# Kernel tuning notes

Hardware: AMD Instinct MI355X
Metric: run time of the kernel (lower is better)

The kernel has to match this reference:

```python
import jax, jax.numpy as jnp
import numpy as np

N = 50000        # nodes
E = 800000       # edges
F_IN = 32        # float features (x also carries 1 trailing cell-id column)
CELL_DIM = 16
NUM_CELLS = 854
C = 64           # out_channels
H0, H1 = 2, 1    # heads schedule for num_layers=2 -> [2, 1]
D_IN = F_IN + CELL_DIM  # 48, GAT input dim after cell embedding concat
NEG_SLOPE = 0.2  # PyG GATConv default negative_slope


def setup_inputs() -> dict:
    key = jax.random.key(0)
    ks = jax.random.split(key, 14)
    base = jax.random.normal(ks[0], (N, F_IN), jnp.float32)
    cell_ids = jax.random.randint(ks[1], (N,), 0, NUM_CELLS)
    x = jnp.concatenate([base, cell_ids.astype(jnp.float32)[:, None]], axis=1)
    edge_index = jax.random.randint(ks[2], (2, E), 0, N, dtype=jnp.int32)
    s = lambda f: 1.0 / np.sqrt(f)
    emb = jax.random.normal(ks[3], (NUM_CELLS, CELL_DIM), jnp.float32)
    W0 = jax.random.normal(ks[4], (D_IN, H0 * C), jnp.float32) * s(D_IN)
    a_src0 = jax.random.normal(ks[5], (H0, C), jnp.float32) * s(C)
    a_dst0 = jax.random.normal(ks[6], (H0, C), jnp.float32) * s(C)
    b0 = jnp.zeros((C,), jnp.float32)
    ln_g = jnp.ones((C,), jnp.float32)
    ln_b = jnp.zeros((C,), jnp.float32)
    W1 = jax.random.normal(ks[7], (C, H1 * C), jnp.float32) * s(C)
    a_src1 = jax.random.normal(ks[8], (H1, C), jnp.float32) * s(C)
    a_dst1 = jax.random.normal(ks[9], (H1, C), jnp.float32) * s(C)
    b1 = jnp.zeros((C,), jnp.float32)
    return {"x": x, "edge_index": edge_index, "emb": emb,
            "W0": W0, "a_src0": a_src0, "a_dst0": a_dst0, "b0": b0,
            "ln_g": ln_g, "ln_b": ln_b,
            "W1": W1, "a_src1": a_src1, "a_dst1": a_dst1, "b1": b1}


def gat_layer(h_in, src, dst, W, a_src, a_dst, b, heads):
    # h_in: [N, D]; src/dst: [E'] (self-loops already appended)
    h = (h_in @ W).reshape(N, heads, C)                 # [N, H, C]
    alpha_s = jnp.einsum('nhc,hc->nh', h, a_src)        # [N, H]
    alpha_d = jnp.einsum('nhc,hc->nh', h, a_dst)
    e = jax.nn.leaky_relu(alpha_s[src] + alpha_d[dst], NEG_SLOPE)  # [E', H]
    # segment softmax over incoming edges of each dst node
    m = jax.ops.segment_max(e, dst, num_segments=N)     # [N, H]
    ex = jnp.exp(e - m[dst])
    denom = jax.ops.segment_sum(ex, dst, num_segments=N)
    alpha = ex / denom[dst]                             # [E', H]
    msg = h[src] * alpha[:, :, None]                    # [E', H, C]
    out = jax.ops.segment_sum(msg, dst, num_segments=N) # [N, H, C]
    return out.mean(axis=1) + b                         # concat=False -> mean over heads


def layer_norm(x, g, b):
    mu = x.mean(-1, keepdims=True)
    var = ((x - mu) ** 2).mean(-1, keepdims=True)
    return (x - mu) * jax.lax.rsqrt(var + 1e-5) * g + b


def reference(x, edge_index, emb, W0, a_src0, a_dst0, b0, ln_g, ln_b,
              W1, a_src1, a_dst1, b1):
    base = x[:, :-1]
    cell_ids = x[:, -1].astype(jnp.int32)
    h = jnp.concatenate([base, emb[cell_ids]], axis=1)  # [N, 48]
    # add self-loops (PyG GATConv default add_self_loops=True)
    loop = jnp.arange(N, dtype=edge_index.dtype)
    src = jnp.concatenate([edge_index[0], loop])
    dst = jnp.concatenate([edge_index[1], loop])
    h = gat_layer(h, src, dst, W0, a_src0, a_dst0, b0, H0)
    h = jax.nn.elu(layer_norm(h, ln_g, ln_b))           # dropout is identity at eval
    h = gat_layer(h, src, dst, W1, a_src1, a_dst1, b1, H1)
    return h
```

## Files before the change

kernel.cpp:

```cpp
#include <hip/hip_runtime.h>
#include <hip/hip_bf16.h>

#define N_NODES 50000
#define N_EDGES 800000
#define F_IN 32
#define CELL_DIM 16
#define D_IN 48
#define X_STRIDE 33
#define NUM_CELLS 854
#define NEG_SLOPE 0.2f
#define NODE0_BLOCKS 2048
#define EDGE_BLOCKS 3125
#define NXCD 8
#define BWX 16
#define W 24

typedef unsigned int uint;
typedef unsigned short ushort;

static __device__ __forceinline__ uint f2b(float f) {
  uint x = __float_as_uint(f);
  return (x + 0x7fffu + ((x >> 16) & 1u)) >> 16;
}
static __device__ __forceinline__ float b2f_lo(uint w) { return __uint_as_float(w << 16); }
static __device__ __forceinline__ float b2f_hi(uint w) { return __uint_as_float(w & 0xffff0000u); }
static __device__ __forceinline__ float lrelu(float e) { return fmaxf(e, NEG_SLOPE * e); }


__global__ __launch_bounds__(256) void k_node0(const float* __restrict__ x,
                                               const float* __restrict__ emb,
                                               const float* __restrict__ W0,
                                               const float* __restrict__ asrc,
                                               const float* __restrict__ adst,
                                               ushort* __restrict__ h0u,
                                               float* __restrict__ as0, float* __restrict__ ad0) {
  int tid = threadIdx.x;
  __shared__ float hin[8][48];
  int lane = tid & 63, wid = tid >> 6;
  int h = wid & 1;
  int q = wid >> 1;
  float w0r[D_IN];
#pragma unroll
  for (int k = 0; k < D_IN; ++k) w0r[k] = W0[k * 128 + h * 64 + lane];
  float av_s = asrc[h * 64 + lane], av_d = adst[h * 64 + lane];

  for (int g = blockIdx.x; g < N_NODES / 8; g += NODE0_BLOCKS) {
    int nb = g * 8;
#pragma unroll
    for (int j = 0; j < 2; ++j) {
      int loc = 2 * wid + j;
      int n = nb + loc;
      float t = 0.f;
      if (lane < 33) t = x[n * X_STRIDE + lane];
      int cid = (int)__shfl(t, 32, 64);
      cid = cid < 0 ? 0 : (cid >= NUM_CELLS ? NUM_CELLS - 1 : cid);
      if (lane >= 32 && lane < 48) t = emb[cid * CELL_DIM + (lane - 32)];
      if (lane < 48) hin[loc][lane] = t;
    }
    __syncthreads();
#pragma unroll
    for (int j = 0; j < 4; ++j) {
      int loc = 4 * q + j;
      int n = nb + loc;
      const float4* hp = (const float4*)hin[loc];
      float acc = 0.f;
#pragma unroll
      for (int k4 = 0; k4 < 12; ++k4) {
        float4 hh = hp[k4];
        acc = fmaf(hh.x, w0r[4 * k4 + 0], acc);
        acc = fmaf(hh.y, w0r[4 * k4 + 1], acc);
        acc = fmaf(hh.z, w0r[4 * k4 + 2], acc);
        acc = fmaf(hh.w, w0r[4 * k4 + 3], acc);
      }
      h0u[(n * 64 + lane) * 2 + h] = (ushort)f2b(acc);
      float sa = acc * av_s, sd = acc * av_d;
#pragma unroll
      for (int o = 32; o >= 1; o >>= 1) {
        sa += __shfl_xor(sa, o, 64);
        sd += __shfl_xor(sd, o, 64);
      }
      if (lane == 0) {
        as0[n * 2 + h] = sa;
        ad0[n * 2 + h] = sd;
      }
    }
    __syncthreads();
  }
}


__global__ __launch_bounds__(256) void k_bfill(const int* __restrict__ ei,
                                               int* __restrict__ cnt,
                                               ushort* __restrict__ bkt) {
  int e = blockIdx.x * 256 + threadIdx.x;
  if (e >= N_EDGES) return;
  uint xcc;
  asm volatile("s_getreg_b32 %0, hwreg(HW_REG_XCC_ID)" : "=s"(xcc));
  xcc &= (NXCD - 1);
  int s = ei[e], d = ei[N_EDGES + e];
  int p = atomicAdd(&cnt[xcc * N_NODES + d], 1);
  if (p < BWX) bkt[(xcc * N_NODES + d) * BWX + p] = (ushort)s;
}



__global__ __launch_bounds__(256) void k_agg0(const int* __restrict__ cnt,
                                              const ushort* __restrict__ bkt,
                                              const float2* __restrict__ as0v,
                                              const float2* __restrict__ ad0v,
                                              const uint* __restrict__ h0p,
                                              const float* __restrict__ b0,
                                              const float* __restrict__ lng,
                                              const float* __restrict__ lnb,
                                              const float* __restrict__ W1,
                                              const float* __restrict__ asrc1,
                                              const float* __restrict__ adst1,
                                              ushort* __restrict__ h1b,
                                              float* __restrict__ as1, float* __restrict__ ad1) {
  __shared__ uint gbuf[4][W * 64];
  __shared__ float yb[4][64];
  int tid = threadIdx.x;
  int lane = tid & 63, wl = tid >> 6;
  int n = blockIdx.x * 4 + wl;
  int cx = 0;
  if (lane < 8) cx = min(cnt[lane * N_NODES + n], BWX);
  int sc = cx;
#pragma unroll
  for (int o = 1; o < 8; o <<= 1) {
    int t = __shfl_up(sc, o, 64);
    if (lane >= o) sc += t;
  }
  int p1 = __shfl(sc, 0, 64), p2 = __shfl(sc, 1, 64), p3 = __shfl(sc, 2, 64);
  int p4 = __shfl(sc, 3, 64), p5 = __shfl(sc, 4, 64), p6 = __shfl(sc, 5, 64);
  int p7 = __shfl(sc, 6, 64);
  int total = __shfl(sc, 7, 64);
  int items = total + 1;

  float2 ad = ad0v[n];
  float acc0 = 0.f, acc1 = 0.f, den0 = 0.f, den1 = 0.f;
  uint* gb = gbuf[wl];

  for (int w0 = 0; w0 < items; w0 += W) {
    int idx = w0 + lane;
    int xsl = (idx >= p1) + (idx >= p2) + (idx >= p3) + (idx >= p4) +
              (idx >= p5) + (idx >= p6) + (idx >= p7);
    int base = xsl == 0 ? 0 : (xsl == 1 ? p1 : (xsl == 2 ? p2 : (xsl == 3 ? p3 :
               (xsl == 4 ? p4 : (xsl == 5 ? p5 : (xsl == 6 ? p6 : p7))))));
    uint sl = (uint)bkt[xsl * (N_NODES * BWX) + n * BWX + (idx - base)];
    uint s = (idx < total) ? sl : (uint)n;
    float wv0 = 0.f, wv1 = 0.f;
    if (lane < W && idx < items) {
      float2 a = as0v[s];
      wv0 = __expf(lrelu(a.x + ad.x));
      wv1 = __expf(lrelu(a.y + ad.y));
    }
#pragma unroll
    for (int j = 0; j < W; ++j) {
      uint sx = (uint)__builtin_amdgcn_readlane((int)s, j);
      __builtin_amdgcn_global_load_lds((const uint*)(h0p + sx * 64u + (uint)lane),
                                       gb + j * 64, 4, 0, 0);
    }
    asm volatile("s_waitcnt vmcnt(0)" ::: "memory");
    __builtin_amdgcn_sched_barrier(0);
#pragma unroll
    for (int j = 0; j < W; ++j) {
      float w0j = __uint_as_float(
          (uint)__builtin_amdgcn_readlane((int)__float_as_uint(wv0), j));
      float w1j = __uint_as_float(
          (uint)__builtin_amdgcn_readlane((int)__float_as_uint(wv1), j));
      uint h = gb[j * 64 + lane];
      acc0 = fmaf(w0j, b2f_lo(h), acc0); den0 += w0j;
      acc1 = fmaf(w1j, b2f_hi(h), acc1); den1 += w1j;
    }
    asm volatile("s_waitcnt lgkmcnt(0)" ::: "memory");
    __builtin_amdgcn_sched_barrier(0);
  }

  float v = 0.5f * (acc0 / den0 + acc1 / den1) + b0[lane];
  float mu = v;
#pragma unroll
  for (int o = 32; o >= 1; o >>= 1) mu += __shfl_xor(mu, o, 64);
  mu *= (1.0f / 64.0f);
  float d = v - mu;
  float vr = d * d;
#pragma unroll
  for (int o = 32; o >= 1; o >>= 1) vr += __shfl_xor(vr, o, 64);
  vr *= (1.0f / 64.0f);
  float y = d * rsqrtf(vr + 1e-5f) * lng[lane] + lnb[lane];
  y = y > 0.f ? y : expm1f(y);
  yb[wl][lane] = y;
  const float4* yp = (const float4*)yb[wl];
  float q0 = 0.f, q1 = 0.f, q2 = 0.f, q3 = 0.f;
#pragma unroll
  for (int k4 = 0; k4 < 16; ++k4) {
    float4 yy = yp[k4];
    q0 = fmaf(yy.x, W1[(4 * k4 + 0) * 64 + lane], q0);
    q1 = fmaf(yy.y, W1[(4 * k4 + 1) * 64 + lane], q1);
    q2 = fmaf(yy.z, W1[(4 * k4 + 2) * 64 + lane], q2);
    q3 = fmaf(yy.w, W1[(4 * k4 + 3) * 64 + lane], q3);
  }
  float h1v = (q0 + q1) + (q2 + q3);
  h1b[n * 64 + lane] = (ushort)f2b(h1v);
  float sa = h1v * asrc1[lane];
  float sdv = h1v * adst1[lane];
#pragma unroll
  for (int o = 32; o >= 1; o >>= 1) {
    sa += __shfl_xor(sa, o, 64);
    sdv += __shfl_xor(sdv, o, 64);
  }
  if (lane == 0) {
    as1[n] = sa;
    ad1[n] = sdv;
  }
}


__global__ __launch_bounds__(256) void k_agg1(const int* __restrict__ cnt,
                                              const ushort* __restrict__ bkt,
                                              const ushort* __restrict__ h1b,
                                              const float* __restrict__ as1,
                                              const float* __restrict__ ad1,
                                              const float* __restrict__ b1,
                                              float* __restrict__ out) {
  __shared__ uint gbuf[4][W * 64];
  int tid = threadIdx.x;
  int lane = tid & 63, wl = tid >> 6;
  int n = blockIdx.x * 4 + wl;
  int cx = 0;
  if (lane < 8) cx = min(cnt[lane * N_NODES + n], BWX);
  int sc = cx;
#pragma unroll
  for (int o = 1; o < 8; o <<= 1) {
    int t = __shfl_up(sc, o, 64);
    if (lane >= o) sc += t;
  }
  int p1 = __shfl(sc, 0, 64), p2 = __shfl(sc, 1, 64), p3 = __shfl(sc, 2, 64);
  int p4 = __shfl(sc, 3, 64), p5 = __shfl(sc, 4, 64), p6 = __shfl(sc, 5, 64);
  int p7 = __shfl(sc, 6, 64);
  int total = __shfl(sc, 7, 64);
  int items = total + 1;

  float adv = ad1[n];
  float acc = 0.f, den = 0.f;
  uint* gb = gbuf[wl];
  const ushort* gbs = (const ushort*)gb;

  for (int w0 = 0; w0 < items; w0 += W) {
    int idx = w0 + lane;
    int xsl = (idx >= p1) + (idx >= p2) + (idx >= p3) + (idx >= p4) +
              (idx >= p5) + (idx >= p6) + (idx >= p7);
    int base = xsl == 0 ? 0 : (xsl == 1 ? p1 : (xsl == 2 ? p2 : (xsl == 3 ? p3 :
               (xsl == 4 ? p4 : (xsl == 5 ? p5 : (xsl == 6 ? p6 : p7))))));
    uint sl = (uint)bkt[xsl * (N_NODES * BWX) + n * BWX + (idx - base)];
    uint s = (idx < total) ? sl : (uint)n;
    float wv = 0.f;
    if (lane < W && idx < items) {
      wv = __expf(lrelu(as1[s] + adv));
    }
    uint hl = lane & 31;
#pragma unroll
    for (int j = 0; j < W; ++j) {
      uint sx = (uint)__builtin_amdgcn_readlane((int)s, j);
      __builtin_amdgcn_global_load_lds((const uint*)(h1b + sx * 64u) + hl,
                                       gb + j * 64, 4, 0, 0);
    }
    asm volatile("s_waitcnt vmcnt(0)" ::: "memory");
    __builtin_amdgcn_sched_barrier(0);
#pragma unroll
    for (int j = 0; j < W; ++j) {
      float wj = __uint_as_float(
          (uint)__builtin_amdgcn_readlane((int)__float_as_uint(wv), j));
      uint hh = (uint)gbs[j * 128 + lane];
      acc = fmaf(wj, __uint_as_float(hh << 16), acc);
      den += wj;
    }
    asm volatile("s_waitcnt lgkmcnt(0)" ::: "memory");
    __builtin_amdgcn_sched_barrier(0);
  }
  out[n * 64 + lane] = acc / den + b1[lane];
}


extern "C" void kernel_launch(void* const* d_in, const int* in_sizes, int n_in,
                              void* d_out, int out_size, void* d_ws, size_t ws_size,
                              hipStream_t stream) {
  const float* x    = (const float*)d_in[0];
  const int*   ei   = (const int*)d_in[1];
  const float* emb  = (const float*)d_in[2];
  const float* W0   = (const float*)d_in[3];
  const float* as0w = (const float*)d_in[4];
  const float* ad0w = (const float*)d_in[5];
  const float* b0   = (const float*)d_in[6];
  const float* lng  = (const float*)d_in[7];
  const float* lnb  = (const float*)d_in[8];
  const float* W1   = (const float*)d_in[9];
  const float* as1w = (const float*)d_in[10];
  const float* ad1w = (const float*)d_in[11];
  const float* b1   = (const float*)d_in[12];
  float* out = (float*)d_out;

  ushort* bkt = (ushort*)d_ws;
  int* cnt   = (int*)(bkt + NXCD * N_NODES * BWX);
  float* as0 = (float*)(cnt + NXCD * N_NODES);
  float* ad0 = as0 + N_NODES * 2;
  float* as1 = ad0 + N_NODES * 2;
  float* ad1 = as1 + N_NODES;
  uint* h0p  = (uint*)(ad1 + N_NODES);
  ushort* h1b = (ushort*)(h0p + N_NODES * 64);

  hipMemsetAsync(cnt, 0, NXCD * N_NODES * sizeof(int), stream);
  k_bfill<<<EDGE_BLOCKS, 256, 0, stream>>>(ei, cnt, bkt);
  k_node0<<<NODE0_BLOCKS, 256, 0, stream>>>(x, emb, W0, as0w, ad0w, (ushort*)h0p, as0, ad0);
  k_agg0<<<N_NODES / 4, 256, 0, stream>>>(cnt, bkt, (const float2*)as0, (const float2*)ad0,
                                          h0p, b0, lng, lnb, W1, as1w, ad1w, h1b, as1, ad1);
  k_agg1<<<N_NODES / 4, 256, 0, stream>>>(cnt, bkt, h1b, as1, ad1, b1, out);
}
```

Baseline: 256.7 us.

## Compact per-XCD edge buckets into a single CSR-like list inside node0 kernel

Adds extra blocks to the node0 kernel that merge the eight per-XCD bucket lists into one compact per-node list of up to 48 sources with a single count. Both aggregation kernels then read that compact list directly instead of doing an 8-way prefix scan and slot selection on every node. This removes repeated scan and indexing work from two kernels at the cost of an extra merge pass with scattered 2-byte writes. Nodes with more than 48 incoming edges would have the excess dropped, where the old code capped each XCD bucket at 16.

```diff
diff --git a/kernel.cpp b/kernel.cpp
--- a/kernel.cpp
+++ b/kernel.cpp
@@ -10,9 +10,11 @@
 #define NUM_CELLS 854
 #define NEG_SLOPE 0.2f
 #define NODE0_BLOCKS 2048
+#define MERGE_BLOCKS 1563
 #define EDGE_BLOCKS 3125
 #define NXCD 8
 #define BWX 16
+#define BW 48
 #define W 24
 
 typedef unsigned int uint;
@@ -25,68 +27,6 @@
 static __device__ __forceinline__ float b2f_lo(uint w) { return __uint_as_float(w << 16); }
 static __device__ __forceinline__ float b2f_hi(uint w) { return __uint_as_float(w & 0xffff0000u); }
 static __device__ __forceinline__ float lrelu(float e) { return fmaxf(e, NEG_SLOPE * e); }
-
-
-__global__ __launch_bounds__(256) void k_node0(const float* __restrict__ x,
-                                               const float* __restrict__ emb,
-                                               const float* __restrict__ W0,
-                                               const float* __restrict__ asrc,
-                                               const float* __restrict__ adst,
-                                               ushort* __restrict__ h0u,
-                                               float* __restrict__ as0, float* __restrict__ ad0) {
-  int tid = threadIdx.x;
-  __shared__ float hin[8][48];
-  int lane = tid & 63, wid = tid >> 6;
-  int h = wid & 1;
-  int q = wid >> 1;
-  float w0r[D_IN];
-#pragma unroll
-  for (int k = 0; k < D_IN; ++k) w0r[k] = W0[k * 128 + h * 64 + lane];
-  float av_s = asrc[h * 64 + lane], av_d = adst[h * 64 + lane];
-
-  for (int g = blockIdx.x; g < N_NODES / 8; g += NODE0_BLOCKS) {
-    int nb = g * 8;
-#pragma unroll
-    for (int j = 0; j < 2; ++j) {
-      int loc = 2 * wid + j;
-      int n = nb + loc;
-      float t = 0.f;
-      if (lane < 33) t = x[n * X_STRIDE + lane];
-      int cid = (int)__shfl(t, 32, 64);
-      cid = cid < 0 ? 0 : (cid >= NUM_CELLS ? NUM_CELLS - 1 : cid);
-      if (lane >= 32 && lane < 48) t = emb[cid * CELL_DIM + (lane - 32)];
-      if (lane < 48) hin[loc][lane] = t;
-    }
-    __syncthreads();
-#pragma unroll
-    for (int j = 0; j < 4; ++j) {
-      int loc = 4 * q + j;
-      int n = nb + loc;
-      const float4* hp = (const float4*)hin[loc];
-      float acc = 0.f;
-#pragma unroll
-      for (int k4 = 0; k4 < 12; ++k4) {
-        float4 hh = hp[k4];
-        acc = fmaf(hh.x, w0r[4 * k4 + 0], acc);
-        acc = fmaf(hh.y, w0r[4 * k4 + 1], acc);
-        acc = fmaf(hh.z, w0r[4 * k4 + 2], acc);
-        acc = fmaf(hh.w, w0r[4 * k4 + 3], acc);
-      }
-      h0u[(n * 64 + lane) * 2 + h] = (ushort)f2b(acc);
-      float sa = acc * av_s, sd = acc * av_d;
-#pragma unroll
-      for (int o = 32; o >= 1; o >>= 1) {
-        sa += __shfl_xor(sa, o, 64);
-        sd += __shfl_xor(sd, o, 64);
-      }
-      if (lane == 0) {
-        as0[n * 2 + h] = sa;
-        ad0[n * 2 + h] = sd;
-      }
-    }
-    __syncthreads();
-  }
-}
 
 
 __global__ __launch_bounds__(256) void k_bfill(const int* __restrict__ ei,
@@ -102,6 +42,92 @@
   if (p < BWX) bkt[(xcc * N_NODES + d) * BWX + p] = (ushort)s;
 }
 
+
+__global__ __launch_bounds__(256) void k_node0(const float* __restrict__ x,
+                                               const float* __restrict__ emb,
+                                               const float* __restrict__ W0,
+                                               const float* __restrict__ asrc,
+                                               const float* __restrict__ adst,
+                                               const int* __restrict__ cnt,
+                                               const ushort* __restrict__ bkt,
+                                               ushort* __restrict__ h0u,
+                                               float* __restrict__ as0, float* __restrict__ ad0,
+                                               int* __restrict__ cntc,
+                                               ushort* __restrict__ bktc) {
+  int tid = threadIdx.x;
+  if (blockIdx.x >= NODE0_BLOCKS) {
+    int n = (blockIdx.x - NODE0_BLOCKS) * 32 + (tid >> 3);
+    if (n >= N_NODES) return;
+    int xg = tid & 7;
+    int cx = min(cnt[xg * N_NODES + n], BWX);
+    int sc = cx;
+#pragma unroll
+    for (int o = 1; o < 8; o <<= 1) {
+      int t = __shfl_up(sc, o, 64);
+      if ((tid & 7) >= o) sc += t;
+    }
+    int total = __shfl(sc, (tid & 63) | 7, 64);
+    int base = sc - cx;
+    const ushort* src = bkt + (xg * N_NODES + n) * BWX;
+    for (int k = 0; k < cx; ++k) {
+      int slot = base + k;
+      if (slot < BW) bktc[n * BW + slot] = src[k];
+    }
+    if (xg == 7) cntc[n] = min(total, BW);
+    return;
+  }
+  __shared__ float hin[8][48];
+  int lane = tid & 63, wid = tid >> 6;
+  int h = wid & 1;
+  int q = wid >> 1;
+  float w0r[D_IN];
+#pragma unroll
+  for (int k = 0; k < D_IN; ++k) w0r[k] = W0[k * 128 + h * 64 + lane];
+  float av_s = asrc[h * 64 + lane], av_d = adst[h * 64 + lane];
+
+  for (int g = blockIdx.x; g < N_NODES / 8; g += NODE0_BLOCKS) {
+    int nb = g * 8;
+#pragma unroll
+    for (int j = 0; j < 2; ++j) {
+      int loc = 2 * wid + j;
+      int n = nb + loc;
+      float t = 0.f;
+      if (lane < 33) t = x[n * X_STRIDE + lane];
+      int cid = (int)__shfl(t, 32, 64);
+      cid = cid < 0 ? 0 : (cid >= NUM_CELLS ? NUM_CELLS - 1 : cid);
+      if (lane >= 32 && lane < 48) t = emb[cid * CELL_DIM + (lane - 32)];
+      if (lane < 48) hin[loc][lane] = t;
+    }
+    __syncthreads();
+#pragma unroll
+    for (int j = 0; j < 4; ++j) {
+      int loc = 4 * q + j;
+      int n = nb + loc;
+      const float4* hp = (const float4*)hin[loc];
+      float acc = 0.f;
+#pragma unroll
+      for (int k4 = 0; k4 < 12; ++k4) {
+        float4 hh = hp[k4];
+        acc = fmaf(hh.x, w0r[4 * k4 + 0], acc);
+        acc = fmaf(hh.y, w0r[4 * k4 + 1], acc);
+        acc = fmaf(hh.z, w0r[4 * k4 + 2], acc);
+        acc = fmaf(hh.w, w0r[4 * k4 + 3], acc);
+      }
+      h0u[(n * 64 + lane) * 2 + h] = (ushort)f2b(acc);
+      float sa = acc * av_s, sd = acc * av_d;
+#pragma unroll
+      for (int o = 32; o >= 1; o >>= 1) {
+        sa += __shfl_xor(sa, o, 64);
+        sd += __shfl_xor(sd, o, 64);
+      }
+      if (lane == 0) {
+        as0[n * 2 + h] = sa;
+        ad0[n * 2 + h] = sd;
+      }
+    }
+    __syncthreads();
+  }
+}
 
 
 __global__ __launch_bounds__(256) void k_agg0(const int* __restrict__ cnt,
@@ -122,34 +148,18 @@
   int tid = threadIdx.x;
   int lane = tid & 63, wl = tid >> 6;
   int n = blockIdx.x * 4 + wl;
-  int cx = 0;
-  if (lane < 8) cx = min(cnt[lane * N_NODES + n], BWX);
-  int sc = cx;
-#pragma unroll
-  for (int o = 1; o < 8; o <<= 1) {
-    int t = __shfl_up(sc, o, 64);
-    if (lane >= o) sc += t;
-  }
-  int p1 = __shfl(sc, 0, 64), p2 = __shfl(sc, 1, 64), p3 = __shfl(sc, 2, 64);
-  int p4 = __shfl(sc, 3, 64), p5 = __shfl(sc, 4, 64), p6 = __shfl(sc, 5, 64);
-  int p7 = __shfl(sc, 6, 64);
-  int total = __shfl(sc, 7, 64);
-  int items = total + 1;
-
+  int nE = cnt[n];
+  int items = nE + 1;
   float2 ad = ad0v[n];
   float acc0 = 0.f, acc1 = 0.f, den0 = 0.f, den1 = 0.f;
   uint* gb = gbuf[wl];
 
   for (int w0 = 0; w0 < items; w0 += W) {
     int idx = w0 + lane;
-    int xsl = (idx >= p1) + (idx >= p2) + (idx >= p3) + (idx >= p4) +
-              (idx >= p5) + (idx >= p6) + (idx >= p7);
-    int base = xsl == 0 ? 0 : (xsl == 1 ? p1 : (xsl == 2 ? p2 : (xsl == 3 ? p3 :
-               (xsl == 4 ? p4 : (xsl == 5 ? p5 : (xsl == 6 ? p6 : p7))))));
-    uint sl = (uint)bkt[xsl * (N_NODES * BWX) + n * BWX + (idx - base)];
-    uint s = (idx < total) ? sl : (uint)n;
+    uint s = 0u;
     float wv0 = 0.f, wv1 = 0.f;
     if (lane < W && idx < items) {
+      s = (idx < nE) ? (uint)bkt[n * BW + idx] : (uint)n;
       float2 a = as0v[s];
       wv0 = __expf(lrelu(a.x + ad.x));
       wv1 = __expf(lrelu(a.y + ad.y));
@@ -226,20 +236,8 @@
   int tid = threadIdx.x;
   int lane = tid & 63, wl = tid >> 6;
   int n = blockIdx.x * 4 + wl;
-  int cx = 0;
-  if (lane < 8) cx = min(cnt[lane * N_NODES + n], BWX);
-  int sc = cx;
-#pragma unroll
-  for (int o = 1; o < 8; o <<= 1) {
-    int t = __shfl_up(sc, o, 64);
-    if (lane >= o) sc += t;
-  }
-  int p1 = __shfl(sc, 0, 64), p2 = __shfl(sc, 1, 64), p3 = __shfl(sc, 2, 64);
-  int p4 = __shfl(sc, 3, 64), p5 = __shfl(sc, 4, 64), p6 = __shfl(sc, 5, 64);
-  int p7 = __shfl(sc, 6, 64);
-  int total = __shfl(sc, 7, 64);
-  int items = total + 1;
-
+  int nE = cnt[n];
+  int items = nE + 1;
   float adv = ad1[n];
   float acc = 0.f, den = 0.f;
   uint* gb = gbuf[wl];
@@ -247,14 +245,10 @@
 
   for (int w0 = 0; w0 < items; w0 += W) {
     int idx = w0 + lane;
-    int xsl = (idx >= p1) + (idx >= p2) + (idx >= p3) + (idx >= p4) +
-              (idx >= p5) + (idx >= p6) + (idx >= p7);
-    int base = xsl == 0 ? 0 : (xsl == 1 ? p1 : (xsl == 2 ? p2 : (xsl == 3 ? p3 :
-               (xsl == 4 ? p4 : (xsl == 5 ? p5 : (xsl == 6 ? p6 : p7))))));
-    uint sl = (uint)bkt[xsl * (N_NODES * BWX) + n * BWX + (idx - base)];
-    uint s = (idx < total) ? sl : (uint)n;
+    uint s = 0u;
     float wv = 0.f;
     if (lane < W && idx < items) {
+      s = (idx < nE) ? (uint)bkt[n * BW + idx] : (uint)n;
       wv = __expf(lrelu(as1[s] + adv));
     }
     uint hl = lane & 31;
@@ -300,8 +294,10 @@
   float* out = (float*)d_out;
 
   ushort* bkt = (ushort*)d_ws;
-  int* cnt   = (int*)(bkt + NXCD * N_NODES * BWX);
-  float* as0 = (float*)(cnt + NXCD * N_NODES);
+  int* cnt    = (int*)(bkt + NXCD * N_NODES * BWX);
+  ushort* bktc = (ushort*)(cnt + NXCD * N_NODES);
+  int* cntc   = (int*)(bktc + N_NODES * BW);
+  float* as0 = (float*)(cntc + N_NODES);
   float* ad0 = as0 + N_NODES * 2;
   float* as1 = ad0 + N_NODES * 2;
   float* ad1 = as1 + N_NODES;
@@ -310,8 +306,9 @@
 
   hipMemsetAsync(cnt, 0, NXCD * N_NODES * sizeof(int), stream);
   k_bfill<<<EDGE_BLOCKS, 256, 0, stream>>>(ei, cnt, bkt);
-  k_node0<<<NODE0_BLOCKS, 256, 0, stream>>>(x, emb, W0, as0w, ad0w, (ushort*)h0p, as0, ad0);
-  k_agg0<<<N_NODES / 4, 256, 0, stream>>>(cnt, bkt, (const float2*)as0, (const float2*)ad0,
+  k_node0<<<NODE0_BLOCKS + MERGE_BLOCKS, 256, 0, stream>>>(x, emb, W0, as0w, ad0w, cnt, bkt,
+                                                           (ushort*)h0p, as0, ad0, cntc, bktc);
+  k_agg0<<<N_NODES / 4, 256, 0, stream>>>(cntc, bktc, (const float2*)as0, (const float2*)ad0,
                                           h0p, b0, lng, lnb, W1, as1w, ad1w, h1b, as1, ad1);
-  k_agg1<<<N_NODES / 4, 256, 0, stream>>>(cnt, bkt, h1b, as1, ad1, b1, out);
-}
+  k_agg1<<<N_NODES / 4, 256, 0, stream>>>(cntc, bktc, h1b, as1, ad1, b1, out);
+}
```

After: 251.9 us. No clear change (-1.9%).
